# Kernel optimization log

Measured on AMD Instinct MI355X. Metric: run time of the kernel, lower is better.

Reference implementation:

```python
import jax, jax.numpy as jnp
import numpy as np

B, N, C = 2, 30, 320
FH = FW = 64          # feature map (latent 128 / downsample 2)
PH = PW = 32          # roi_scale output size at this level
ORIG = 128.0          # original (latent) spatial size
SCALE = 0.5           # spatial_scale = 1/downsample_rate
SR = 2                # sampling_ratio
M = N + 1             # global channel + rois


def _bilinear(img, y, x):
    # img: (C, H, W); y, x: arbitrary-shape float coords. torchvision-style:
    # zero outside [-1, H]/[ -1, W], clamp then 4-corner interp.
    H, W = img.shape[1], img.shape[2]
    valid = (y > -1.0) & (y < H) & (x > -1.0) & (x < W)
    yc = jnp.clip(y, 0.0, H - 1.0)
    xc = jnp.clip(x, 0.0, W - 1.0)
    y0 = jnp.floor(yc).astype(jnp.int32)
    x0 = jnp.floor(xc).astype(jnp.int32)
    y1 = jnp.minimum(y0 + 1, H - 1)
    x1 = jnp.minimum(x0 + 1, W - 1)
    wy = yc - y0
    wx = xc - x0
    v = (img[:, y0, x0] * (1 - wy) * (1 - wx)
         + img[:, y0, x1] * (1 - wy) * wx
         + img[:, y1, x0] * wy * (1 - wx)
         + img[:, y1, x1] * wy * wx)
    return v * valid


def _roi_align_one(img, x1, y1, bw, bh):
    # img (C,FH,FW); x1,y1,bw,bh (N,) in aligned feature coords / bin sizes
    s = (jnp.arange(PH * SR, dtype=img.dtype) + 0.5) / SR   # sub-sample offsets in bin units
    yy = y1[:, None] + s[None, :] * bh[:, None]             # (N, PH*SR)
    xx = x1[:, None] + s[None, :] * bw[:, None]             # (N, PW*SR)
    yg = jnp.broadcast_to(yy[:, :, None], (N, PH * SR, PW * SR))
    xg = jnp.broadcast_to(xx[:, None, :], (N, PH * SR, PW * SR))
    v = _bilinear(img, yg, xg)                              # (C, N, PH*SR, PW*SR)
    v = v.reshape(C, N, PH, SR, PW, SR).mean(axis=(3, 5))   # average sub-samples
    return v.transpose(1, 0, 2, 3)                          # (N, C, PH, PW)


def _roi_unpool_one(roi_imgs, x1, y1, bw, bh):
    # inverse of roi_align: paste each (C,PH,PW) roi back into its own (FH,FW) map
    ys = jnp.arange(FH, dtype=roi_imgs.dtype)
    xs = jnp.arange(FW, dtype=roi_imgs.dtype)
    ry = (ys[None, :] - y1[:, None]) / bh[:, None] - 0.5    # (N, FH) roi-grid coords
    rx = (xs[None, :] - x1[:, None]) / bw[:, None] - 0.5    # (N, FW)
    ryg = jnp.broadcast_to(ry[:, :, None], (N, FH, FW))
    rxg = jnp.broadcast_to(rx[:, None, :], (N, FH, FW))
    return jax.vmap(_bilinear)(roi_imgs, ryg, rxg)          # (N, C, FH, FW); zeros outside box


def _fuser(x, perm, w_reduce, w1, b1, w2, b2):
    # FuseWeightGenerator: x (B, M, C, H, W)
    fg = jnp.sum(x, axis=2) != 0                            # (B, M, H, W) foreground mask
    fw = jnp.einsum('bmchw,c->bmhw', x, w_reduce)           # 1x1 conv C->1, no bias
    g = fw[:, :1]
    r = fw[:, 1:][:, perm]                                  # shuffle roi channels
    gin = jnp.concatenate([g, r], axis=1)                   # (B, M, H, W)
    # ChannelGate: only the 'max' branch affects the output (original uses last channel_att_raw)
    mp = gin.max(axis=(2, 3))                               # (B, M)
    att = jax.nn.relu(mp @ w1 + b1) @ w2 + b2
    gated = gin * jax.nn.sigmoid(att)[:, :, None, None]
    inv = jnp.argsort(perm)
    fw = jnp.concatenate([gated[:, :1], gated[:, 1:][:, inv]], axis=1)
    fw = jnp.where(fg, fw, jnp.finfo(fw.dtype).min)
    w = jax.nn.softmax(fw, axis=1)[:, :, None]              # (B, M, 1, H, W)
    return jnp.sum(x * w, axis=1)                           # (B, C, H, W)


def _forward(normed_hidden_states, attn_output, instance_boxes, instance_masks, perm,
             w_reduce, w1, b1, w2, b2):
    fmap = normed_hidden_states.reshape(B, FH, FW, C).transpose(0, 3, 1, 2)  # b c h w
    boxes = instance_boxes * ORIG * SCALE - 0.5             # aligned=True feature coords
    x1, y1 = boxes[..., 0], boxes[..., 1]
    x2, y2 = boxes[..., 2], boxes[..., 3]
    bw = (x2 - x1) / PW
    bh = (y2 - y1) / PH
    roi_feats = jax.vmap(_roi_align_one)(fmap, x1, y1, bw, bh)   # (B,N,C,PH,PW)
    mask = instance_masks.astype(roi_feats.dtype)[:, :, None, None, None]
    roi_feats = roi_feats * mask                             # masked rois stay zero
    unpooled = jax.vmap(_roi_unpool_one)(roi_feats, x1, y1, bw, bh) * mask  # (B,N,C,FH,FW)
    attn_map = attn_output.reshape(B, FH, FW, C).transpose(0, 3, 1, 2)[:, None]
    x = jnp.concatenate([attn_map, unpooled], axis=1)        # (B, M, C, FH, FW)
    fused = _fuser(x, perm, w_reduce, w1, b1, w2, b2)        # (B, C, FH, FW)
    return fused.transpose(0, 2, 3, 1).reshape(B, FH * FW, C)


def setup_inputs() -> dict:
    key = jax.random.key(0)
    ks = jax.random.split(key, 10)
    nhs = jax.random.normal(ks[0], (B, FH * FW, C), dtype=jnp.float32)
    attn = jax.random.normal(ks[1], (B, FH * FW, C), dtype=jnp.float32)
    cx = jax.random.uniform(ks[2], (B, N), minval=0.25, maxval=0.75)
    cy = jax.random.uniform(ks[3], (B, N), minval=0.25, maxval=0.75)
    hw = jax.random.uniform(ks[4], (B, N, 2), minval=0.1, maxval=0.4)
    boxes = jnp.stack([cx - hw[..., 0] / 2, cy - hw[..., 1] / 2,
                       cx + hw[..., 0] / 2, cy + hw[..., 1] / 2], axis=-1)
    boxes = jnp.clip(boxes, 0.0, 1.0).astype(jnp.float32)    # normalized xyxy
    masks = jax.random.randint(ks[5], (B, N), 0, 2).astype(jnp.int32)
    perm = jax.random.permutation(ks[6], N).astype(jnp.int32)
    w_reduce = (jax.random.normal(ks[7], (C,), dtype=jnp.float32) / np.sqrt(C)).astype(jnp.float32)
    w1 = (jax.random.normal(ks[8], (M, M), dtype=jnp.float32) / np.sqrt(M)).astype(jnp.float32)
    b1 = jnp.zeros((M,), dtype=jnp.float32)
    w2 = (jax.random.normal(ks[9], (M, M), dtype=jnp.float32) / np.sqrt(M)).astype(jnp.float32)
    b2 = jnp.zeros((M,), dtype=jnp.float32)
    return {"normed_hidden_states": nhs, "attn_output": attn, "instance_boxes": boxes,
            "instance_masks": masks, "perm": perm, "w_reduce": w_reduce,
            "w1": w1, "b1": b1, "w2": w2, "b2": b2}


def reference(normed_hidden_states, attn_output, instance_boxes, instance_masks, perm,
              w_reduce, w1, b1, w2, b2):
    return _forward(normed_hidden_states, attn_output, instance_boxes, instance_masks, perm,
                    w_reduce, w1, b1, w2, b2)
```

## Files before the change

kernel.cpp:

```cpp
#include <hip/hip_runtime.h>
#include <hip/hip_bf16.h>

#define NB 2
#define NN 30
#define NC 320
#define NM 31
#define HW 4096
#define FMIN_F (-3.40282346638528859812e+38f)

typedef float nfloat4 __attribute__((ext_vector_type(4)));

#define OFF_FSUM   0
#define OFF_FWRED  8192
#define OFF_ASUM   16384
#define OFF_AWRED  24576
#define OFF_Z      32768
#define OFF_MP     286720
#define OFF_AMSK   286784
#define OFF_WGT    294976
#define WS_FLOATS  548928

__device__ __forceinline__ void get_box(const float* boxes, int b, int n,
                                        float& x1, float& y1, float& bw, float& bh) {
    const float* p = boxes + (b * NN + n) * 4;
    float X1 = p[0] * 64.0f - 0.5f;
    float Y1 = p[1] * 64.0f - 0.5f;
    float X2 = p[2] * 64.0f - 0.5f;
    float Y2 = p[3] * 64.0f - 0.5f;
    x1 = X1; y1 = Y1;
    bw = (X2 - X1) / 32.0f;
    bh = (Y2 - Y1) / 32.0f;
}

__device__ __forceinline__ unsigned short f2bf(float f) {
    __hip_bfloat16 h = __float2bfloat16(f);
    return *reinterpret_cast<unsigned short*>(&h);
}
__device__ __forceinline__ float bf2f(unsigned short u) {
    return __uint_as_float(((unsigned int)u) << 16);
}

__global__ void k_reduce(const float* __restrict__ nhs, const float* __restrict__ attn,
                         const float* __restrict__ wred, float* __restrict__ ws) {
    int wave = threadIdx.x >> 6;
    int lane = threadIdx.x & 63;
    int row = blockIdx.x * 4 + wave;
    const float4* n4 = (const float4*)(nhs + (size_t)row * NC);
    const float4* a4 = (const float4*)(attn + (size_t)row * NC);
    const float4* w4 = (const float4*)wred;
    float4 wv = w4[lane];
    float4 nv = n4[lane];
    float4 av = a4[lane];
    float s_n = nv.x + nv.y + nv.z + nv.w;
    float w_n = nv.x * wv.x + nv.y * wv.y + nv.z * wv.z + nv.w * wv.w;
    float s_a = av.x + av.y + av.z + av.w;
    float w_a = av.x * wv.x + av.y * wv.y + av.z * wv.z + av.w * wv.w;
    if (lane < 16) {
        float4 wv2 = w4[lane + 64];
        float4 nv2 = n4[lane + 64];
        float4 av2 = a4[lane + 64];
        s_n += nv2.x + nv2.y + nv2.z + nv2.w;
        w_n += nv2.x * wv2.x + nv2.y * wv2.y + nv2.z * wv2.z + nv2.w * wv2.w;
        s_a += av2.x + av2.y + av2.z + av2.w;
        w_a += av2.x * wv2.x + av2.y * wv2.y + av2.z * wv2.z + av2.w * wv2.w;
    }
#pragma unroll
    for (int off = 32; off > 0; off >>= 1) {
        s_n += __shfl_down(s_n, off, 64);
        w_n += __shfl_down(w_n, off, 64);
        s_a += __shfl_down(s_a, off, 64);
        w_a += __shfl_down(w_a, off, 64);
    }
    if (lane == 0) {
        ws[OFF_FSUM + row]  = s_n;
        ws[OFF_FWRED + row] = w_n;
        ws[OFF_ASUM + row]  = s_a;
        ws[OFF_AWRED + row] = w_a;
    }
}

__global__ void k_fw(const float* __restrict__ boxes, const int* __restrict__ masks,
                     float* __restrict__ ws) {
    int bm = blockIdx.x;
    int b = bm / NM, m = bm % NM;
    __shared__ float rs[1024], rw[1024];
    __shared__ float red[256];
    float locmax = -INFINITY;
    int tid = threadIdx.x;
    if (m == 0) {
        for (int pix = tid; pix < HW; pix += 256) {
            float fwv = ws[OFF_AWRED + b * HW + pix];
            bool fg = (ws[OFF_ASUM + b * HW + pix] != 0.0f);
            ws[OFF_Z + (size_t)bm * HW + pix] = fg ? fwv : FMIN_F;
            locmax = fmaxf(locmax, fwv);
        }
    } else {
        int n = m - 1;
        int msk = masks[b * NN + n];
        if (msk) {
            float x1, y1, bw, bh;
            get_box(boxes, b, n, x1, y1, bw, bh);
            const float* fsum  = ws + OFF_FSUM + b * HW;
            const float* fwred = ws + OFF_FWRED + b * HW;
            for (int cell = tid; cell < 1024; cell += 256) {
                int q = cell & 31, p = cell >> 5;
                float accs = 0.f, accw = 0.f;
#pragma unroll
                for (int di = 0; di < 2; di++) {
#pragma unroll
                    for (int dj = 0; dj < 2; dj++) {
                        float y = y1 + ((float)p + 0.25f + 0.5f * (float)di) * bh;
                        float x = x1 + ((float)q + 0.25f + 0.5f * (float)dj) * bw;
                        bool valid = (y > -1.0f) && (y < 64.0f) && (x > -1.0f) && (x < 64.0f);
                        if (valid) {
                            float yc = fminf(fmaxf(y, 0.0f), 63.0f);
                            float xc = fminf(fmaxf(x, 0.0f), 63.0f);
                            int iy0 = (int)floorf(yc), ix0 = (int)floorf(xc);
                            int iy1 = min(iy0 + 1, 63), ix1 = min(ix0 + 1, 63);
                            float wy = yc - (float)iy0, wx = xc - (float)ix0;
                            float w00 = (1.f - wy) * (1.f - wx), w01 = (1.f - wy) * wx;
                            float w10 = wy * (1.f - wx), w11 = wy * wx;
                            accs += w00 * fsum[iy0 * 64 + ix0] + w01 * fsum[iy0 * 64 + ix1]
                                  + w10 * fsum[iy1 * 64 + ix0] + w11 * fsum[iy1 * 64 + ix1];
                            accw += w00 * fwred[iy0 * 64 + ix0] + w01 * fwred[iy0 * 64 + ix1]
                                  + w10 * fwred[iy1 * 64 + ix0] + w11 * fwred[iy1 * 64 + ix1];
                        }
                    }
                }
                rs[cell] = accs * 0.25f;
                rw[cell] = accw * 0.25f;
            }
            __syncthreads();
            for (int pix = tid; pix < HW; pix += 256) {
                int h = pix >> 6, wp = pix & 63;
                float fwv = 0.0f;
                bool fg = false;
                float ry = ((float)h - y1) / bh - 0.5f;
                float rx = ((float)wp - x1) / bw - 0.5f;
                bool valid = (ry > -1.0f) && (ry < 32.0f) && (rx > -1.0f) && (rx < 32.0f);
                if (valid) {
                    float yc = fminf(fmaxf(ry, 0.0f), 31.0f);
                    float xc = fminf(fmaxf(rx, 0.0f), 31.0f);
                    int iy0 = (int)floorf(yc), ix0 = (int)floorf(xc);
                    int iy1 = min(iy0 + 1, 31), ix1 = min(ix0 + 1, 31);
                    float wy = yc - (float)iy0, wx = xc - (float)ix0;
                    float w00 = (1.f - wy) * (1.f - wx), w01 = (1.f - wy) * wx;
                    float w10 = wy * (1.f - wx), w11 = wy * wx;
                    fwv = w00 * rw[iy0 * 32 + ix0] + w01 * rw[iy0 * 32 + ix1]
                        + w10 * rw[iy1 * 32 + ix0] + w11 * rw[iy1 * 32 + ix1];
                    float su = w00 * rs[iy0 * 32 + ix0] + w01 * rs[iy0 * 32 + ix1]
                             + w10 * rs[iy1 * 32 + ix0] + w11 * rs[iy1 * 32 + ix1];
                    fg = (su != 0.0f);
                }
                ws[OFF_Z + (size_t)bm * HW + pix] = fg ? fwv : FMIN_F;
                locmax = fmaxf(locmax, fwv);
            }
        } else {
            for (int pix = tid; pix < HW; pix += 256)
                ws[OFF_Z + (size_t)bm * HW + pix] = FMIN_F;
            locmax = 0.0f;
        }
    }
    red[tid] = locmax;
    __syncthreads();
    for (int s = 128; s > 0; s >>= 1) {
        if (tid < s) red[tid] = fmaxf(red[tid], red[tid + s]);
        __syncthreads();
    }
    if (tid == 0) ws[OFF_MP + bm] = red[0];
}

__global__ void k_soft(const int* __restrict__ perm, const float* __restrict__ w1,
                       const float* __restrict__ b1, const float* __restrict__ w2,
                       const float* __restrict__ b2, float* __restrict__ ws) {
    __shared__ float mpg[NB][NM], hb[NB][NM], scal[NB][NM];
    int t = threadIdx.x;
    if (t < NB * NM) {
        int b = t / NM, j = t % NM;
        float v = (j == 0) ? ws[OFF_MP + b * NM]
                           : ws[OFF_MP + b * NM + 1 + perm[j - 1]];
        mpg[b][j] = v;
    }
    __syncthreads();
    if (t < NB * NM) {
        int b = t / NM, j = t % NM;
        float a = b1[j];
        for (int k = 0; k < NM; k++) a += mpg[b][k] * w1[k * NM + j];
        hb[b][j] = fmaxf(a, 0.0f);
    }
    __syncthreads();
    if (t < NB * NM) {
        int b = t / NM, j = t % NM;
        float a = b2[j];
        for (int k = 0; k < NM; k++) a += hb[b][k] * w2[k * NM + j];
        float sig = 1.0f / (1.0f + expf(-a));
        if (j == 0) scal[b][0] = sig;
        else        scal[b][1 + perm[j - 1]] = sig;
    }
    __syncthreads();

    int idx = blockIdx.x * 256 + t;
    int b = idx >> 12, pix = idx & 4095;
    float z[NM];
    float mx = -INFINITY;
#pragma unroll
    for (int m = 0; m < NM; m++) {
        float v = ws[OFF_Z + ((size_t)(b * NM + m)) * HW + pix];
        float zz = (v == FMIN_F) ? FMIN_F : v * scal[b][m];
        z[m] = zz;
        mx = fmaxf(mx, zz);
    }
    float sum = 0.0f;
#pragma unroll
    for (int m = 0; m < NM; m++) {
        float e = expf(z[m] - mx);
        z[m] = e;
        sum += e;
    }
    float inv = 1.0f / sum;
    unsigned amask = 0u;
#pragma unroll
    for (int m = 0; m < NM; m++) {
        float w = z[m] * inv;
        ws[OFF_WGT + m * (NB * HW) + idx] = w;
        if (m >= 1 && w != 0.0f) amask |= (1u << (m - 1));
    }
    ((unsigned*)(ws + OFF_AMSK))[idx] = amask;
}

__global__ void k_roifeat(const float* __restrict__ nhs, const float* __restrict__ boxes,
                          const int* __restrict__ masks, unsigned short* __restrict__ roif) {
    int bn = blockIdx.x >> 8;
    int n = bn % NN;
    int b = bn / NN;
    if (masks[b * NN + n] == 0) return;
    int tid = threadIdx.x;
    int cid = tid / 80;
    int v = tid - cid * 80;
    int cell = blockIdx.x * 4 + cid;
    int q = cell & 31;
    int p = (cell >> 5) & 31;
    float x1, y1, bw, bh;
    get_box(boxes, b, n, x1, y1, bw, bh);
    float wc[4][4];
    int ic[4][4];
    bool vv[4];
#pragma unroll
    for (int s_ = 0; s_ < 4; s_++) {
        int di = s_ >> 1, dj = s_ & 1;
        float y = y1 + ((float)p + 0.25f + 0.5f * (float)di) * bh;
        float x = x1 + ((float)q + 0.25f + 0.5f * (float)dj) * bw;
        vv[s_] = (y > -1.0f) && (y < 64.0f) && (x > -1.0f) && (x < 64.0f);
        float yc = fminf(fmaxf(y, 0.0f), 63.0f);
        float xc = fminf(fmaxf(x, 0.0f), 63.0f);
        int iy0 = (int)floorf(yc), ix0 = (int)floorf(xc);
        int iy1 = min(iy0 + 1, 63), ix1 = min(ix0 + 1, 63);
        float wy = yc - (float)iy0, wx = xc - (float)ix0;
        wc[s_][0] = (1.f - wy) * (1.f - wx);
        wc[s_][1] = (1.f - wy) * wx;
        wc[s_][2] = wy * (1.f - wx);
        wc[s_][3] = wy * wx;
        ic[s_][0] = iy0 * 64 + ix0;
        ic[s_][1] = iy0 * 64 + ix1;
        ic[s_][2] = iy1 * 64 + ix0;
        ic[s_][3] = iy1 * 64 + ix1;
    }
    const float4* fb4 = (const float4*)(nhs + (size_t)b * HW * NC);
    float4 acc = make_float4(0.f, 0.f, 0.f, 0.f);
#pragma unroll
    for (int s_ = 0; s_ < 4; s_++) {
        if (vv[s_]) {
#pragma unroll
            for (int t_ = 0; t_ < 4; t_++) {
                float w = wc[s_][t_];
                float4 fv = fb4[ic[s_][t_] * 80 + v];
                acc.x += w * fv.x; acc.y += w * fv.y;
                acc.z += w * fv.z; acc.w += w * fv.w;
            }
        }
    }
    ushort4 pk;
    pk.x = f2bf(acc.x * 0.25f);
    pk.y = f2bf(acc.y * 0.25f);
    pk.z = f2bf(acc.z * 0.25f);
    pk.w = f2bf(acc.w * 0.25f);
    ((ushort4*)roif)[(size_t)cell * 80 + v] = pk;
}

__global__ void k_final(const float* __restrict__ attn, const float* __restrict__ boxes,
                        const float* __restrict__ ws, const unsigned short* __restrict__ roif,
                        float* __restrict__ out) {
    int tid = threadIdx.x;
    int pid = tid / 80;
    int v = tid - pid * 80;
    int idx = blockIdx.x * 4 + pid;
    int b = idx >> 12, pix = idx & 4095;
    int h = pix >> 6, wp = pix & 63;
    float w0 = ws[OFF_WGT + idx];
    unsigned amask = ((const unsigned*)(ws + OFF_AMSK))[idx];
    float4 a4 = ((const float4*)attn)[(size_t)idx * 80 + v];
    float4 acc;
    acc.x = a4.x * w0; acc.y = a4.y * w0; acc.z = a4.z * w0; acc.w = a4.w * w0;
    const ushort4* r4 = (const ushort4*)roif;
    while (amask) {
        int n = __ffs(amask) - 1;
        amask &= amask - 1;
        float wn = ws[OFF_WGT + (n + 1) * (NB * HW) + idx];
        float x1, y1, bw, bh;
        get_box(boxes, b, n, x1, y1, bw, bh);
        float ry = ((float)h - y1) / bh - 0.5f;
        float rx = ((float)wp - x1) / bw - 0.5f;
        float yc = fminf(fmaxf(ry, 0.0f), 31.0f);
        float xc = fminf(fmaxf(rx, 0.0f), 31.0f);
        int iy0 = (int)floorf(yc), ix0 = (int)floorf(xc);
        int iy1 = min(iy0 + 1, 31), ix1 = min(ix0 + 1, 31);
        float wy = yc - (float)iy0, wx = xc - (float)ix0;
        float w00 = (1.f - wy) * (1.f - wx) * wn, w01 = (1.f - wy) * wx * wn;
        float w10 = wy * (1.f - wx) * wn, w11 = wy * wx * wn;
        size_t base = ((size_t)(b * NN + n)) << 10;
        ushort4 u00 = r4[(base + iy0 * 32 + ix0) * 80 + v];
        ushort4 u01 = r4[(base + iy0 * 32 + ix1) * 80 + v];
        ushort4 u10 = r4[(base + iy1 * 32 + ix0) * 80 + v];
        ushort4 u11 = r4[(base + iy1 * 32 + ix1) * 80 + v];
        acc.x += w00 * bf2f(u00.x) + w01 * bf2f(u01.x) + w10 * bf2f(u10.x) + w11 * bf2f(u11.x);
        acc.y += w00 * bf2f(u00.y) + w01 * bf2f(u01.y) + w10 * bf2f(u10.y) + w11 * bf2f(u11.y);
        acc.z += w00 * bf2f(u00.z) + w01 * bf2f(u01.z) + w10 * bf2f(u10.z) + w11 * bf2f(u11.z);
        acc.w += w00 * bf2f(u00.w) + w01 * bf2f(u01.w) + w10 * bf2f(u10.w) + w11 * bf2f(u11.w);
    }
    nfloat4 nv = { acc.x, acc.y, acc.z, acc.w };
    __builtin_nontemporal_store(nv, ((nfloat4*)out) + (size_t)idx * 80 + v);
}

extern "C" void kernel_launch(void* const* d_in, const int* in_sizes, int n_in,
                              void* d_out, int out_size, void* d_ws, size_t ws_size,
                              hipStream_t stream) {
    const float* nhs   = (const float*)d_in[0];
    const float* attn  = (const float*)d_in[1];
    const float* boxes = (const float*)d_in[2];
    const int*   masks = (const int*)d_in[3];
    const int*   perm  = (const int*)d_in[4];
    const float* wred  = (const float*)d_in[5];
    const float* w1    = (const float*)d_in[6];
    const float* b1    = (const float*)d_in[7];
    const float* w2    = (const float*)d_in[8];
    const float* b2    = (const float*)d_in[9];
    float* out = (float*)d_out;
    float* ws = (float*)d_ws;
    unsigned short* roif = (unsigned short*)((char*)d_ws + (size_t)WS_FLOATS * 4);

    k_roifeat<<<NB * NN * 256, 320, 0, stream>>>(nhs, boxes, masks, roif);
    k_reduce<<<2048, 256, 0, stream>>>(nhs, attn, wred, ws);
    k_fw<<<NB * NM, 256, 0, stream>>>(boxes, masks, ws);
    k_soft<<<32, 256, 0, stream>>>(perm, w1, b1, w2, b2, ws);
    k_final<<<NB * HW / 4, 320, 0, stream>>>(attn, boxes, ws, roif, out);
}
```

Baseline: 142.4 us.

## Merge roifeat and reduce into one launch; fold softmax into final kernel

Combines the ROI-align feature kernel and the row-reduction kernel into a single launch that dispatches on block index, with the reduce part now using 5 waves of the 320-thread blocks. The MLP-gating and per-pixel softmax are moved into k_final, computed per block in shared memory with warp shuffles, so the weight and active-mask buffers in workspace are no longer written and read back. This removes two launches and a global round-trip. In exchange, every final block recomputes the tiny 31x31 MLP, and the loop now scans all 30 rois instead of a precomputed bitmask.

```diff
diff --git a/kernel.cpp b/kernel.cpp
--- a/kernel.cpp
+++ b/kernel.cpp
@@ -16,9 +16,10 @@
 #define OFF_AWRED  24576
 #define OFF_Z      32768
 #define OFF_MP     286720
-#define OFF_AMSK   286784
-#define OFF_WGT    294976
-#define WS_FLOATS  548928
+#define WS_FLOATS  286784
+
+#define GRID_ROIF (NB * NN * 256)
+#define GRID_RED  1639
 
 __device__ __forceinline__ void get_box(const float* boxes, int b, int n,
                                         float& x1, float& y1, float& bw, float& bh) {
@@ -40,11 +41,74 @@
     return __uint_as_float(((unsigned int)u) << 16);
 }
 
-__global__ void k_reduce(const float* __restrict__ nhs, const float* __restrict__ attn,
-                         const float* __restrict__ wred, float* __restrict__ ws) {
+__device__ void do_roifeat(int blk, const float* __restrict__ nhs,
+                           const float* __restrict__ boxes,
+                           const int* __restrict__ masks,
+                           unsigned short* __restrict__ roif) {
+    int bn = blk >> 8;
+    int n = bn % NN;
+    int b = bn / NN;
+    if (masks[b * NN + n] == 0) return;
+    int tid = threadIdx.x;
+    int cid = tid / 80;
+    int v = tid - cid * 80;
+    int cell = blk * 4 + cid;
+    int q = cell & 31;
+    int p = (cell >> 5) & 31;
+    float x1, y1, bw, bh;
+    get_box(boxes, b, n, x1, y1, bw, bh);
+    float wc[4][4];
+    int ic[4][4];
+    bool vv[4];
+#pragma unroll
+    for (int s_ = 0; s_ < 4; s_++) {
+        int di = s_ >> 1, dj = s_ & 1;
+        float y = y1 + ((float)p + 0.25f + 0.5f * (float)di) * bh;
+        float x = x1 + ((float)q + 0.25f + 0.5f * (float)dj) * bw;
+        vv[s_] = (y > -1.0f) && (y < 64.0f) && (x > -1.0f) && (x < 64.0f);
+        float yc = fminf(fmaxf(y, 0.0f), 63.0f);
+        float xc = fminf(fmaxf(x, 0.0f), 63.0f);
+        int iy0 = (int)floorf(yc), ix0 = (int)floorf(xc);
+        int iy1 = min(iy0 + 1, 63), ix1 = min(ix0 + 1, 63);
+        float wy = yc - (float)iy0, wx = xc - (float)ix0;
+        wc[s_][0] = (1.f - wy) * (1.f - wx);
+        wc[s_][1] = (1.f - wy) * wx;
+        wc[s_][2] = wy * (1.f - wx);
+        wc[s_][3] = wy * wx;
+        ic[s_][0] = iy0 * 64 + ix0;
+        ic[s_][1] = iy0 * 64 + ix1;
+        ic[s_][2] = iy1 * 64 + ix0;
+        ic[s_][3] = iy1 * 64 + ix1;
+    }
+    const float4* fb4 = (const float4*)(nhs + (size_t)b * HW * NC);
+    float4 acc = make_float4(0.f, 0.f, 0.f, 0.f);
+#pragma unroll
+    for (int s_ = 0; s_ < 4; s_++) {
+        if (vv[s_]) {
+#pragma unroll
+            for (int t_ = 0; t_ < 4; t_++) {
+                float w = wc[s_][t_];
+                float4 fv = fb4[ic[s_][t_] * 80 + v];
+                acc.x += w * fv.x; acc.y += w * fv.y;
+                acc.z += w * fv.z; acc.w += w * fv.w;
+            }
+        }
+    }
+    ushort4 pk;
+    pk.x = f2bf(acc.x * 0.25f);
+    pk.y = f2bf(acc.y * 0.25f);
+    pk.z = f2bf(acc.z * 0.25f);
+    pk.w = f2bf(acc.w * 0.25f);
+    ((ushort4*)roif)[(size_t)cell * 80 + v] = pk;
+}
+
+__device__ void do_reduce(int rblk, const float* __restrict__ nhs,
+                          const float* __restrict__ attn,
+                          const float* __restrict__ wred, float* __restrict__ ws) {
     int wave = threadIdx.x >> 6;
     int lane = threadIdx.x & 63;
-    int row = blockIdx.x * 4 + wave;
+    int row = rblk * 5 + wave;
+    if (row >= NB * HW) return;
     const float4* n4 = (const float4*)(nhs + (size_t)row * NC);
     const float4* a4 = (const float4*)(attn + (size_t)row * NC);
     const float4* w4 = (const float4*)wred;
@@ -76,6 +140,18 @@
         ws[OFF_FWRED + row] = w_n;
         ws[OFF_ASUM + row]  = s_a;
         ws[OFF_AWRED + row] = w_a;
+    }
+}
+
+__global__ void k_stage1(const float* __restrict__ nhs, const float* __restrict__ attn,
+                         const float* __restrict__ boxes, const int* __restrict__ masks,
+                         const float* __restrict__ wred, float* __restrict__ ws,
+                         unsigned short* __restrict__ roif) {
+    int blk = blockIdx.x;
+    if (blk < GRID_ROIF) {
+        do_roifeat(blk, nhs, boxes, masks, roif);
+    } else {
+        do_reduce(blk - GRID_ROIF, nhs, attn, wred, ws);
     }
 }
 
@@ -170,142 +246,72 @@
     if (tid == 0) ws[OFF_MP + bm] = red[0];
 }
 
-__global__ void k_soft(const int* __restrict__ perm, const float* __restrict__ w1,
-                       const float* __restrict__ b1, const float* __restrict__ w2,
-                       const float* __restrict__ b2, float* __restrict__ ws) {
-    __shared__ float mpg[NB][NM], hb[NB][NM], scal[NB][NM];
+__global__ void k_final(const float* __restrict__ attn, const float* __restrict__ boxes,
+                        const int* __restrict__ perm, const float* __restrict__ w1,
+                        const float* __restrict__ b1, const float* __restrict__ w2,
+                        const float* __restrict__ b2, const float* __restrict__ ws,
+                        const unsigned short* __restrict__ roif, float* __restrict__ out) {
+    __shared__ float mpg[NM], hb[NM], scal[32], wbuf[4][32];
     int t = threadIdx.x;
-    if (t < NB * NM) {
-        int b = t / NM, j = t % NM;
-        float v = (j == 0) ? ws[OFF_MP + b * NM]
-                           : ws[OFF_MP + b * NM + 1 + perm[j - 1]];
-        mpg[b][j] = v;
-    }
-    __syncthreads();
-    if (t < NB * NM) {
-        int b = t / NM, j = t % NM;
-        float a = b1[j];
-        for (int k = 0; k < NM; k++) a += mpg[b][k] * w1[k * NM + j];
-        hb[b][j] = fmaxf(a, 0.0f);
-    }
-    __syncthreads();
-    if (t < NB * NM) {
-        int b = t / NM, j = t % NM;
-        float a = b2[j];
-        for (int k = 0; k < NM; k++) a += hb[b][k] * w2[k * NM + j];
+    int idx0 = blockIdx.x * 4;
+    int b = idx0 >> 12;
+
+    if (t < NM) {
+        mpg[t] = (t == 0) ? ws[OFF_MP + b * NM]
+                          : ws[OFF_MP + b * NM + 1 + perm[t - 1]];
+    }
+    __syncthreads();
+    if (t < NM) {
+        float a = b1[t];
+#pragma unroll
+        for (int k = 0; k < NM; k++) a += mpg[k] * w1[k * NM + t];
+        hb[t] = fmaxf(a, 0.0f);
+    }
+    __syncthreads();
+    if (t < NM) {
+        float a = b2[t];
+#pragma unroll
+        for (int k = 0; k < NM; k++) a += hb[k] * w2[k * NM + t];
         float sig = 1.0f / (1.0f + expf(-a));
-        if (j == 0) scal[b][0] = sig;
-        else        scal[b][1 + perm[j - 1]] = sig;
-    }
-    __syncthreads();
-
-    int idx = blockIdx.x * 256 + t;
-    int b = idx >> 12, pix = idx & 4095;
-    float z[NM];
-    float mx = -INFINITY;
-#pragma unroll
-    for (int m = 0; m < NM; m++) {
-        float v = ws[OFF_Z + ((size_t)(b * NM + m)) * HW + pix];
-        float zz = (v == FMIN_F) ? FMIN_F : v * scal[b][m];
-        z[m] = zz;
-        mx = fmaxf(mx, zz);
-    }
-    float sum = 0.0f;
-#pragma unroll
-    for (int m = 0; m < NM; m++) {
-        float e = expf(z[m] - mx);
-        z[m] = e;
-        sum += e;
-    }
-    float inv = 1.0f / sum;
-    unsigned amask = 0u;
-#pragma unroll
-    for (int m = 0; m < NM; m++) {
-        float w = z[m] * inv;
-        ws[OFF_WGT + m * (NB * HW) + idx] = w;
-        if (m >= 1 && w != 0.0f) amask |= (1u << (m - 1));
-    }
-    ((unsigned*)(ws + OFF_AMSK))[idx] = amask;
-}
-
-__global__ void k_roifeat(const float* __restrict__ nhs, const float* __restrict__ boxes,
-                          const int* __restrict__ masks, unsigned short* __restrict__ roif) {
-    int bn = blockIdx.x >> 8;
-    int n = bn % NN;
-    int b = bn / NN;
-    if (masks[b * NN + n] == 0) return;
-    int tid = threadIdx.x;
-    int cid = tid / 80;
-    int v = tid - cid * 80;
-    int cell = blockIdx.x * 4 + cid;
-    int q = cell & 31;
-    int p = (cell >> 5) & 31;
-    float x1, y1, bw, bh;
-    get_box(boxes, b, n, x1, y1, bw, bh);
-    float wc[4][4];
-    int ic[4][4];
-    bool vv[4];
-#pragma unroll
-    for (int s_ = 0; s_ < 4; s_++) {
-        int di = s_ >> 1, dj = s_ & 1;
-        float y = y1 + ((float)p + 0.25f + 0.5f * (float)di) * bh;
-        float x = x1 + ((float)q + 0.25f + 0.5f * (float)dj) * bw;
-        vv[s_] = (y > -1.0f) && (y < 64.0f) && (x > -1.0f) && (x < 64.0f);
-        float yc = fminf(fmaxf(y, 0.0f), 63.0f);
-        float xc = fminf(fmaxf(x, 0.0f), 63.0f);
-        int iy0 = (int)floorf(yc), ix0 = (int)floorf(xc);
-        int iy1 = min(iy0 + 1, 63), ix1 = min(ix0 + 1, 63);
-        float wy = yc - (float)iy0, wx = xc - (float)ix0;
-        wc[s_][0] = (1.f - wy) * (1.f - wx);
-        wc[s_][1] = (1.f - wy) * wx;
-        wc[s_][2] = wy * (1.f - wx);
-        wc[s_][3] = wy * wx;
-        ic[s_][0] = iy0 * 64 + ix0;
-        ic[s_][1] = iy0 * 64 + ix1;
-        ic[s_][2] = iy1 * 64 + ix0;
-        ic[s_][3] = iy1 * 64 + ix1;
-    }
-    const float4* fb4 = (const float4*)(nhs + (size_t)b * HW * NC);
-    float4 acc = make_float4(0.f, 0.f, 0.f, 0.f);
-#pragma unroll
-    for (int s_ = 0; s_ < 4; s_++) {
-        if (vv[s_]) {
-#pragma unroll
-            for (int t_ = 0; t_ < 4; t_++) {
-                float w = wc[s_][t_];
-                float4 fv = fb4[ic[s_][t_] * 80 + v];
-                acc.x += w * fv.x; acc.y += w * fv.y;
-                acc.z += w * fv.z; acc.w += w * fv.w;
-            }
+        if (t == 0) scal[0] = sig;
+        else        scal[1 + perm[t - 1]] = sig;
+    }
+    __syncthreads();
+
+    if (t < 128) {
+        int pg = t >> 5, m = t & 31;
+        int pix = (idx0 + pg) & 4095;
+        float zz = FMIN_F;
+        if (m < NM) {
+            float v = ws[OFF_Z + (size_t)(b * NM + m) * HW + pix];
+            zz = (v == FMIN_F) ? FMIN_F : v * scal[m];
         }
-    }
-    ushort4 pk;
-    pk.x = f2bf(acc.x * 0.25f);
-    pk.y = f2bf(acc.y * 0.25f);
-    pk.z = f2bf(acc.z * 0.25f);
-    pk.w = f2bf(acc.w * 0.25f);
-    ((ushort4*)roif)[(size_t)cell * 80 + v] = pk;
-}
-
-__global__ void k_final(const float* __restrict__ attn, const float* __restrict__ boxes,
-                        const float* __restrict__ ws, const unsigned short* __restrict__ roif,
-                        float* __restrict__ out) {
-    int tid = threadIdx.x;
-    int pid = tid / 80;
-    int v = tid - pid * 80;
-    int idx = blockIdx.x * 4 + pid;
-    int b = idx >> 12, pix = idx & 4095;
+        float mx = zz;
+#pragma unroll
+        for (int off = 16; off > 0; off >>= 1)
+            mx = fmaxf(mx, __shfl_xor(mx, off, 64));
+        float e = (m < NM) ? expf(zz - mx) : 0.0f;
+        float s = e;
+#pragma unroll
+        for (int off = 16; off > 0; off >>= 1)
+            s += __shfl_xor(s, off, 64);
+        if (m < NM) wbuf[pg][m] = e / s;
+    }
+    __syncthreads();
+
+    int pid = t / 80;
+    int v = t - pid * 80;
+    int idx = idx0 + pid;
+    int pix = idx & 4095;
     int h = pix >> 6, wp = pix & 63;
-    float w0 = ws[OFF_WGT + idx];
-    unsigned amask = ((const unsigned*)(ws + OFF_AMSK))[idx];
+    float w0 = wbuf[pid][0];
     float4 a4 = ((const float4*)attn)[(size_t)idx * 80 + v];
     float4 acc;
     acc.x = a4.x * w0; acc.y = a4.y * w0; acc.z = a4.z * w0; acc.w = a4.w * w0;
     const ushort4* r4 = (const ushort4*)roif;
-    while (amask) {
-        int n = __ffs(amask) - 1;
-        amask &= amask - 1;
-        float wn = ws[OFF_WGT + (n + 1) * (NB * HW) + idx];
+    for (int n = 0; n < NN; n++) {
+        float wn = wbuf[pid][n + 1];
+        if (wn == 0.0f) continue;
         float x1, y1, bw, bh;
         get_box(boxes, b, n, x1, y1, bw, bh);
         float ry = ((float)h - y1) / bh - 0.5f;
@@ -348,9 +354,7 @@
     float* ws = (float*)d_ws;
     unsigned short* roif = (unsigned short*)((char*)d_ws + (size_t)WS_FLOATS * 4);
 
-    k_roifeat<<<NB * NN * 256, 320, 0, stream>>>(nhs, boxes, masks, roif);
-    k_reduce<<<2048, 256, 0, stream>>>(nhs, attn, wred, ws);
+    k_stage1<<<GRID_ROIF + GRID_RED, 320, 0, stream>>>(nhs, attn, boxes, masks, wred, ws, roif);
     k_fw<<<NB * NM, 256, 0, stream>>>(boxes, masks, ws);
-    k_soft<<<32, 256, 0, stream>>>(perm, w1, b1, w2, b2, ws);
-    k_final<<<NB * HW / 4, 320, 0, stream>>>(attn, boxes, ws, roif, out);
-}
+    k_final<<<NB * HW / 4, 320, 0, stream>>>(attn, boxes, perm, w1, b1, w2, b2, ws, roif, out);
+}
```

Measured after the change: 131.6 us. 1.08x faster.
